# Kernel tuning notes

Hardware: AMD Instinct MI355X
Metric: run time of the kernel (lower is better)

Reference implementation:

```python
import jax, jax.numpy as jnp
import numpy as np

B, S, D, H, DQ, DM = 1, 2048, 1024, 16, 64, 4096
EPS = 1e-5
TEMPERATURE = 1.0


def layer_norm(x, gamma, beta):
    m = x.mean(-1, keepdims=True)
    v = jnp.mean((x - m) ** 2, axis=-1, keepdims=True)  # unbiased=False
    return gamma * (x - m) / jnp.sqrt(v + EPS) + beta


def setup_inputs() -> dict:
    key = jax.random.key(0)
    ks = jax.random.split(key, 12)
    w = lambda k, shape: jax.random.normal(k, shape, jnp.float32) * 0.02
    return {
        "E": jax.random.normal(ks[0], (B, S, D), jnp.float32),
        "mask": jnp.tril(jnp.ones((S, S), jnp.int32)),  # causal
        "W_Q": w(ks[1], (D, D)),
        "W_K": w(ks[2], (D, D)),
        "W_V": w(ks[3], (D, D)),
        "W_O": w(ks[4], (D, D)),
        "H_Q": w(ks[5], (H, DQ, D)),  # per-head Linear weights [out,in]
        "H_K": w(ks[6], (H, DQ, D)),
        "H_V": w(ks[7], (H, DQ, D)),
        "L1_w": w(ks[8], (DM, D)),
        "L1_b": jnp.zeros((DM,), jnp.float32),
        "L2_w": w(ks[9], (D, DM)),
        "L2_b": jnp.zeros((D,), jnp.float32),
        "gamma1": jnp.ones((D,), jnp.float32),
        "beta1": jnp.zeros((D,), jnp.float32),
        "gamma2": jnp.ones((D,), jnp.float32),
        "beta2": jnp.zeros((D,), jnp.float32),
    }


def reference(E, mask, W_Q, W_K, W_V, W_O, H_Q, H_K, H_V,
              L1_w, L1_b, L2_w, L2_b, gamma1, beta1, gamma2, beta2):
    # --- multi-head attention (dropout omitted: inference/eval) ---
    Q = E @ W_Q.T  # [B,S,D]
    K = E @ W_K.T
    V = E @ W_V.T
    # per-head projections (vectorized over the torch per-head Linear loop)
    q = jnp.einsum('bsd,hed->bhse', Q, H_Q)  # [B,H,S,DQ]
    k = jnp.einsum('bsd,hed->bhse', K, H_K)
    v = jnp.einsum('bsd,hed->bhse', V, H_V)
    scores = jnp.einsum('bhse,bhte->bhst', q, k) / jnp.sqrt(jnp.float32(DQ))
    scores = jnp.where(mask == 0, jnp.float32(-1e9), scores)
    weights = jax.nn.softmax(scores, axis=-1) / TEMPERATURE
    o = jnp.einsum('bhst,bhte->bhse', weights, v)        # [B,H,S,DQ]
    o = o.transpose(0, 2, 1, 3).reshape(E.shape[0], E.shape[1], D)  # concat heads
    att = o @ W_O.T
    # residual 1: E + Norm(sublayer(E))  (norm applied to sublayer output)
    x1 = E + layer_norm(att, gamma1, beta1)
    # --- MLP ---
    mlp = jax.nn.relu(x1 @ L1_w.T + L1_b) @ L2_w.T + L2_b
    return x1 + layer_norm(mlp, gamma2, beta2)
```

## Files before the change

### kernel.cpp

```cpp
#include <hip/hip_runtime.h>
#include <hip/hip_bf16.h>
#include <stdint.h>
#include <stddef.h>

typedef __attribute__((ext_vector_type(8))) short bf16x8;
typedef __attribute__((ext_vector_type(4))) short short4v;
typedef __attribute__((ext_vector_type(4))) float f32x4;

#define DEV static __device__ __forceinline__

DEV float bf2f(short s) {
  union { unsigned int u; float f; } c;
  c.u = ((unsigned int)(unsigned short)s) << 16;
  return c.f;
}
DEV short f2bf(float f) {
  union { float f; unsigned int u; } c; c.f = f;
  c.u += 0x7fffu + ((c.u >> 16) & 1);
  return (short)(c.u >> 16);
}
DEV unsigned int cvtpk_bf16(float lo, float hi) {
  unsigned int r;
  asm("v_cvt_pk_bf16_f32 %0, %1, %2" : "=v"(r) : "v"(lo), "v"(hi));
  return r;
}

struct CvtJob { const float* src; short* dst; int n4; };
struct CvtArgs { CvtJob j[8]; int n; };

__global__ __launch_bounds__(256) void cvt_kernel(CvtArgs a) {
  int tid = blockIdx.x * blockDim.x + threadIdx.x;
  int stride = gridDim.x * blockDim.x;
  for (int jj = 0; jj < a.n; ++jj) {
    const float4* s = (const float4*)a.j[jj].src;
    short4v* d = (short4v*)a.j[jj].dst;
    int n4 = a.j[jj].n4;
    for (int i = tid; i < n4; i += stride) {
      float4 v = s[i];
      short4v o = { f2bf(v.x), f2bf(v.y), f2bf(v.z), f2bf(v.w) };
      d[i] = o;
    }
  }
}

struct TcvtArgs { const float* src[3]; short* dst[3]; };

__global__ __launch_bounds__(256) void tcvt_kernel(TcvtArgs a) {
  __shared__ float tile[64][65];
  int z = blockIdx.z;
  const float* src = a.src[z];
  short* dst = a.dst[z];
  int bi = blockIdx.x * 64;
  int bj = blockIdx.y * 64;
  int t = threadIdx.x;
  int r0 = t >> 4;
  int c4 = (t & 15) * 4;
  #pragma unroll
  for (int rr = 0; rr < 4; ++rr) {
    int r = rr * 16 + r0;
    float4 v = *(const float4*)&src[(size_t)(bi + r) * 1024 + bj + c4];
    tile[r][c4] = v.x; tile[r][c4 + 1] = v.y; tile[r][c4 + 2] = v.z; tile[r][c4 + 3] = v.w;
  }
  __syncthreads();
  #pragma unroll
  for (int ww = 0; ww < 4; ++ww) {
    int orow = ww * 16 + r0;
    short4v o = { f2bf(tile[c4][orow]), f2bf(tile[c4 + 1][orow]),
                  f2bf(tile[c4 + 2][orow]), f2bf(tile[c4 + 3][orow]) };
    *(short4v*)&dst[(size_t)(bj + orow) * 1024 + bi + c4] = o;
  }
}

struct GemmArgs {
  const short* A[4];
  const short* B[4];
  void* C[4];
  const float* bias;
  int M, N, K, klen, kbase_step;
};

template<int EPI>
__global__ __launch_bounds__(256) void gemm_bt(GemmArgs g) {
  __shared__ alignas(16) short As[2][128 * 64];
  __shared__ alignas(16) short Bs[2][128 * 64];
  int z = blockIdx.z;
  const short* A = g.A[z];
  const short* B = g.B[z];
  int kb = z * g.kbase_step;

  int bx = blockIdx.x, by = blockIdx.y;
  int tid = threadIdx.x;
  int lane = tid & 63, wid = tid >> 6;
  int l15 = lane & 15, l4 = lane >> 4;
  int wr = (wid >> 1) * 64, wc = (wid & 1) * 64;
  int K = g.K, N = g.N;

  const short* Ab = A + (size_t)(by * 128) * K + kb;
  const short* Bb = B + (size_t)(bx * 128) * K + kb;

  int sR = lane >> 3;
  int sC = ((lane & 7) ^ sR) * 8;

  auto stage = [&](int buf, int k0) {
    const short* Abk = Ab + k0;
    const short* Bbk = Bb + k0;
    #pragma unroll
    for (int i = 0; i < 4; ++i) {
      int rbase = (wid * 4 + i) * 8;
      __builtin_amdgcn_global_load_lds(
          (const __attribute__((address_space(1))) void*)(Abk + (size_t)(rbase + sR) * K + sC),
          (__attribute__((address_space(3))) void*)&As[buf][rbase * 64], 16, 0, 0);
      __builtin_amdgcn_global_load_lds(
          (const __attribute__((address_space(1))) void*)(Bbk + (size_t)(rbase + sR) * K + sC),
          (__attribute__((address_space(3))) void*)&Bs[buf][rbase * 64], 16, 0, 0);
    }
  };

  f32x4 acc[4][4] = {};

  stage(0, 0);
  int cur = 0;

  for (int k0 = 0; k0 < g.klen; k0 += 64) {
    if (k0 + 64 < g.klen) {
      stage(cur ^ 1, k0 + 64);
      asm volatile("s_waitcnt vmcnt(8)" ::: "memory");
    } else {
      asm volatile("s_waitcnt vmcnt(0)" ::: "memory");
    }
    __builtin_amdgcn_s_barrier();

    bf16x8 af[2][4], bfr[2][4];
    int rj = l15 & 7;
    #pragma unroll
    for (int kk = 0; kk < 2; ++kk) {
      #pragma unroll
      for (int mi = 0; mi < 4; ++mi) {
        int r = wr + mi * 16 + l15;
        af[kk][mi] = *(const bf16x8*)&As[cur][r * 64 + (((kk << 2) | l4) ^ rj) * 8];
      }
      #pragma unroll
      for (int ni = 0; ni < 4; ++ni) {
        int r = wc + ni * 16 + l15;
        bfr[kk][ni] = *(const bf16x8*)&Bs[cur][r * 64 + (((kk << 2) | l4) ^ rj) * 8];
      }
    }
    #pragma unroll
    for (int kk = 0; kk < 2; ++kk)
      #pragma unroll
      for (int mi = 0; mi < 4; ++mi)
        #pragma unroll
        for (int ni = 0; ni < 4; ++ni)
          acc[mi][ni] = __builtin_amdgcn_mfma_f32_16x16x32_bf16(af[kk][mi], bfr[kk][ni], acc[mi][ni], 0, 0, 0);

    asm volatile("" ::: "memory");
    __builtin_amdgcn_s_barrier();
    cur ^= 1;
  }

  #pragma unroll
  for (int mi = 0; mi < 4; ++mi) {
    #pragma unroll
    for (int ni = 0; ni < 4; ++ni) {
      int col = bx * 128 + wc + ni * 16 + l15;
      float bv = 0.f;
      if (EPI == 1) bv = g.bias[col];
      bool ct = (EPI == 3) || (EPI == 4 && z == 2);
      if (ct) {
        int row0 = by * 128 + wr + mi * 16 + l4 * 4;
        short4v o4 = { f2bf(acc[mi][ni][0]), f2bf(acc[mi][ni][1]),
                       f2bf(acc[mi][ni][2]), f2bf(acc[mi][ni][3]) };
        *(short4v*)&((short*)g.C[z])[(size_t)col * g.M + row0] = o4;
      } else {
        #pragma unroll
        for (int j = 0; j < 4; ++j) {
          int row = by * 128 + wr + mi * 16 + l4 * 4 + j;
          float v = acc[mi][ni][j];
          if (EPI == 0 || EPI == 4) {
            ((short*)g.C[z])[(size_t)row * N + col] = f2bf(v);
          } else if (EPI == 1) {
            v = fmaxf(v + bv, 0.f);
            ((short*)g.C[z])[(size_t)row * N + col] = f2bf(v);
          } else {
            ((float*)g.C[z])[(size_t)row * N + col] = v;
          }
        }
      }
    }
  }
}

__global__ __launch_bounds__(256, 4) void flash_attn(
    const short* __restrict__ q, const short* __restrict__ k,
    const short* __restrict__ vt, short* __restrict__ o,
    float* __restrict__ Opart, float* __restrict__ Ml)
{
  const int HD = 1024, SS = 2048;
  int h = blockIdx.x;
  int cid = blockIdx.y;
  int qb = 0, cx = cid;
  while (cx >= (qb >> 3) + 1) { cx -= (qb >> 3) + 1; ++qb; }
  int nch = (qb >> 3) + 1;
  int tf = cx << 3;
  int tl = min(qb, tf + 7);
  int qbase = qb << 6;

  int tid = threadIdx.x;
  int wid = tid >> 6, lane = tid & 63;
  int l15 = lane & 15, l4 = lane >> 4;

  __shared__ alignas(16) short Ks[2][64 * 64];
  __shared__ alignas(16) short Vs[2][64 * 64];
  __shared__ alignas(16) char PsB[4][2048];

  bf16x8 qf[2];
  {
    int qr = qbase + wid * 16 + l15;
    const short* qp = q + (size_t)qr * HD + h * 64 + l4 * 8;
    bf16x8 r0 = *(const bf16x8*)qp;
    bf16x8 r1 = *(const bf16x8*)(qp + 32);
    const float SC = 0.1803368801f;
    #pragma unroll
    for (int j = 0; j < 8; ++j) {
      qf[0][j] = f2bf(bf2f(r0[j]) * SC);
      qf[1][j] = f2bf(bf2f(r1[j]) * SC);
    }
  }

  int sR = lane >> 3;
  int sC = (lane & 7) ^ sR;

  auto stage = [&](int buf, int t0) {
    const short* kbase = k + (size_t)t0 * HD + h * 64;
    const short* vbase = vt + (size_t)(h * 64) * SS + t0;
    #pragma unroll
    for (int i = 0; i < 2; ++i) {
      int rb = wid * 16 + i * 8;
      __builtin_amdgcn_global_load_lds(
          (const __attribute__((address_space(1))) void*)(kbase + (size_t)(rb + sR) * HD + sC * 8),
          (__attribute__((address_space(3))) void*)&Ks[buf][rb * 64], 16, 0, 0);
      __builtin_amdgcn_global_load_lds(
          (const __attribute__((address_space(1))) void*)(vbase + (size_t)(rb + sR) * SS + sC * 8),
          (__attribute__((address_space(3))) void*)&Vs[buf][rb * 64], 16, 0, 0);
    }
  };

  f32x4 oacc[4] = {};
  float mrun = -1e30f, lrun = 0.f;
  int q_g = qbase + wid * 16 + l15;
  int sbase = (lane & 48) + ((lane & 48) >> 2);

  char* Pw = &PsB[wid][l15 << 7];
  int swz = (l15 & 7) << 4;

  stage(0, tf << 6);
  int cur = 0;

  for (int tt = tf; tt <= tl; ++tt) {
    if (tt < tl) {
      stage(cur ^ 1, (tt + 1) << 6);
      asm volatile("s_waitcnt vmcnt(4)" ::: "memory");
    } else {
      asm volatile("s_waitcnt vmcnt(0)" ::: "memory");
    }
    __builtin_amdgcn_s_barrier();

    const short* KsB = &Ks[cur][0];
    const short* VsB = &Vs[cur][0];
    int t0 = tt << 6;

    f32x4 sc[4] = {};
    __builtin_amdgcn_s_setprio(1);
    #pragma unroll
    for (int ks = 0; ks < 2; ++ks)
      #pragma unroll
      for (int ns = 0; ns < 4; ++ns) {
        int r = ns * 16 + l15;
        bf16x8 kf = *(const bf16x8*)&KsB[r * 64 + (((ks << 2) | l4) ^ (r & 7)) * 8];
        sc[ns] = __builtin_amdgcn_mfma_f32_16x16x32_bf16(kf, qf[ks], sc[ns], 0, 0, 0);
      }
    __builtin_amdgcn_s_setprio(0);

    if (tt == qb) {
      #pragma unroll
      for (int ns = 0; ns < 4; ++ns)
        #pragma unroll
        for (int j = 0; j < 4; ++j) {
          int t_g = t0 + ns * 16 + l4 * 4 + j;
          if (t_g > q_g) sc[ns][j] = -1e30f;
        }
    }

    float mloc = sc[0][0];
    #pragma unroll
    for (int ns = 0; ns < 4; ++ns)
      #pragma unroll
      for (int j = 0; j < 4; ++j) mloc = fmaxf(mloc, sc[ns][j]);
    mloc = fmaxf(mloc, __shfl_xor(mloc, 16, 64));
    mloc = fmaxf(mloc, __shfl_xor(mloc, 32, 64));

    if (!__all(mloc - mrun <= 8.0f)) {
      float mnew = fmaxf(mrun, mloc);
      float sco = exp2f(mrun - mnew);
      float scR[4];
      #pragma unroll
      for (int j = 0; j < 4; ++j) scR[j] = __shfl(sco, sbase + j, 64);
      #pragma unroll
      for (int es = 0; es < 4; ++es)
        #pragma unroll
        for (int j = 0; j < 4; ++j) oacc[es][j] *= scR[j];
      lrun *= sco;
      mrun = mnew;
    }

    float psum = 0.f;
    float p[4][4];
    #pragma unroll
    for (int ns = 0; ns < 4; ++ns)
      #pragma unroll
      for (int j = 0; j < 4; ++j) {
        p[ns][j] = exp2f(sc[ns][j] - mrun);
        psum += p[ns][j];
      }
    psum += __shfl_xor(psum, 16, 64);
    psum += __shfl_xor(psum, 32, 64);
    lrun += psum;

    #pragma unroll
    for (int ns = 0; ns < 4; ++ns) {
      uint2 pv = { cvtpk_bf16(p[ns][0], p[ns][1]), cvtpk_bf16(p[ns][2], p[ns][3]) };
      *(uint2*)&Pw[((ns << 5) | (l4 << 3)) ^ swz] = pv;
    }

    __builtin_amdgcn_s_setprio(1);
    #pragma unroll
    for (int ks = 0; ks < 2; ++ks) {
      bf16x8 pf = *(const bf16x8*)&Pw[((ks << 6) | (l4 << 4)) ^ swz];
      #pragma unroll
      for (int es = 0; es < 4; ++es) {
        int r = es * 16 + l15;
        bf16x8 vf = *(const bf16x8*)&VsB[r * 64 + (((ks << 2) | l4) ^ (r & 7)) * 8];
        oacc[es] = __builtin_amdgcn_mfma_f32_16x16x32_bf16(pf, vf, oacc[es], 0, 0, 0);
      }
    }
    __builtin_amdgcn_s_setprio(0);

    asm volatile("" ::: "memory");
    __builtin_amdgcn_s_barrier();
    cur ^= 1;
  }

  if (nch == 1) {
    float linv = 1.f / lrun;
    float invR[4];
    #pragma unroll
    for (int j = 0; j < 4; ++j) invR[j] = __shfl(linv, sbase + j, 64);
    #pragma unroll
    for (int es = 0; es < 4; ++es)
      #pragma unroll
      for (int j = 0; j < 4; ++j) {
        int row = qbase + wid * 16 + l4 * 4 + j;
        o[(size_t)row * HD + h * 64 + es * 16 + l15] = f2bf(oacc[es][j] * invR[j]);
      }
  } else {
    size_t slot = (size_t)h * 80 + cid;
    float* op = Opart + slot * 4096;
    #pragma unroll
    for (int es = 0; es < 4; ++es)
      #pragma unroll
      for (int j = 0; j < 4; ++j) {
        int row = wid * 16 + l4 * 4 + j;
        op[row * 64 + es * 16 + l15] = oacc[es][j];
      }
    if (l4 == 0) {
      Ml[slot * 128 + wid * 16 + l15] = mrun;
      Ml[slot * 128 + 64 + wid * 16 + l15] = lrun;
    }
  }
}

__global__ __launch_bounds__(256) void attn_combine(
    const float* __restrict__ Opart, const float* __restrict__ Ml,
    short* __restrict__ o)
{
  const int HD = 1024;
  int h = blockIdx.x;
  int qb = 8 + blockIdx.y;
  int nch = (qb >> 3) + 1;
  int cb = 0;
  for (int qq = 0; qq < qb; ++qq) cb += (qq >> 3) + 1;
  int tid = threadIdx.x;
  int r = tid >> 2;
  int cq = (tid & 3) << 4;
  size_t slot0 = (size_t)h * 80 + cb;

  float mk[4], lk[4];
  float M = -1e30f;
  #pragma unroll
  for (int kk = 0; kk < 4; ++kk) {
    bool en = kk < nch;
    mk[kk] = en ? Ml[(slot0 + kk) * 128 + r] : -1e30f;
    lk[kk] = en ? Ml[(slot0 + kk) * 128 + 64 + r] : 0.f;
    M = fmaxf(M, mk[kk]);
  }
  float L = 0.f, w[4];
  #pragma unroll
  for (int kk = 0; kk < 4; ++kk) { w[kk] = exp2f(mk[kk] - M); L += w[kk] * lk[kk]; }

  float acc[16] = {};
  #pragma unroll
  for (int kk = 0; kk < 4; ++kk) {
    if (kk < nch) {
      const float* op = Opart + (slot0 + kk) * 4096 + r * 64 + cq;
      float wk = w[kk];
      #pragma unroll
      for (int c4 = 0; c4 < 4; ++c4) {
        float4 v = *(const float4*)&op[c4 * 4];
        acc[c4 * 4 + 0] += wk * v.x;
        acc[c4 * 4 + 1] += wk * v.y;
        acc[c4 * 4 + 2] += wk * v.z;
        acc[c4 * 4 + 3] += wk * v.w;
      }
    }
  }
  float inv = 1.f / L;
  int orow = (qb << 6) + r;
  short* dst = o + (size_t)orow * HD + h * 64 + cq;
  #pragma unroll
  for (int c4 = 0; c4 < 4; ++c4) {
    short4v ov = { f2bf(acc[c4 * 4 + 0] * inv), f2bf(acc[c4 * 4 + 1] * inv),
                   f2bf(acc[c4 * 4 + 2] * inv), f2bf(acc[c4 * 4 + 3] * inv) };
    *(short4v*)&dst[c4 * 4] = ov;
  }
}

__global__ __launch_bounds__(256) void ln_res1(
    const float* __restrict__ P0, const float* __restrict__ P1,
    const float* __restrict__ P2, const float* __restrict__ P3,
    const float* __restrict__ E,
    const float* __restrict__ gamma, const float* __restrict__ beta,
    float* __restrict__ x1f, short* __restrict__ x1b)
{
  int row = blockIdx.x, tid = threadIdx.x;
  int lane = tid & 63, wid = tid >> 6;
  size_t idx = (size_t)row * 1024 + tid * 4;
  float4 p0 = *(const float4*)&P0[idx];
  float4 p1 = *(const float4*)&P1[idx];
  float4 p2 = *(const float4*)&P2[idx];
  float4 p3 = *(const float4*)&P3[idx];
  float a[4] = { p0.x + p1.x + p2.x + p3.x, p0.y + p1.y + p2.y + p3.y,
                 p0.z + p1.z + p2.z + p3.z, p0.w + p1.w + p2.w + p3.w };
  float s = a[0] + a[1] + a[2] + a[3];
  float q = a[0]*a[0] + a[1]*a[1] + a[2]*a[2] + a[3]*a[3];
  #pragma unroll
  for (int off = 1; off < 64; off <<= 1) { s += __shfl_xor(s, off, 64); q += __shfl_xor(q, off, 64); }
  __shared__ float red[8];
  if (lane == 0) { red[wid] = s; red[4 + wid] = q; }
  __syncthreads();
  s = red[0] + red[1] + red[2] + red[3];
  q = red[4] + red[5] + red[6] + red[7];
  float mean = s * (1.f / 1024.f);
  float var = q * (1.f / 1024.f) - mean * mean;
  float rstd = rsqrtf(var + 1e-5f);
  float4 ev = *(const float4*)&E[idx];
  float4 gv = *(const float4*)&gamma[tid * 4];
  float4 bv = *(const float4*)&beta[tid * 4];
  float o0 = ev.x + gv.x * (a[0] - mean) * rstd + bv.x;
  float o1 = ev.y + gv.y * (a[1] - mean) * rstd + bv.y;
  float o2 = ev.z + gv.z * (a[2] - mean) * rstd + bv.z;
  float o3 = ev.w + gv.w * (a[3] - mean) * rstd + bv.w;
  float4 xo = { o0, o1, o2, o3 };
  *(float4*)&x1f[idx] = xo;
  short4v xb = { f2bf(o0), f2bf(o1), f2bf(o2), f2bf(o3) };
  *(short4v*)&x1b[idx] = xb;
}

__global__ __launch_bounds__(256) void ln_res2(
    const float* __restrict__ M0, const float* __restrict__ M1,
    const float* __restrict__ M2, const float* __restrict__ M3,
    const float* __restrict__ bias, const float* __restrict__ x1f,
    const float* __restrict__ gamma, const float* __restrict__ beta,
    float* __restrict__ out)
{
  int row = blockIdx.x, tid = threadIdx.x;
  int lane = tid & 63, wid = tid >> 6;
  size_t idx = (size_t)row * 1024 + tid * 4;
  float4 m0 = *(const float4*)&M0[idx];
  float4 m1 = *(const float4*)&M1[idx];
  float4 m2 = *(const float4*)&M2[idx];
  float4 m3 = *(const float4*)&M3[idx];
  float4 bb = *(const float4*)&bias[tid * 4];
  float a[4] = { m0.x + m1.x + m2.x + m3.x + bb.x,
                 m0.y + m1.y + m2.y + m3.y + bb.y,
                 m0.z + m1.z + m2.z + m3.z + bb.z,
                 m0.w + m1.w + m2.w + m3.w + bb.w };
  float s = a[0] + a[1] + a[2] + a[3];
  float q = a[0]*a[0] + a[1]*a[1] + a[2]*a[2] + a[3]*a[3];
  #pragma unroll
  for (int off = 1; off < 64; off <<= 1) { s += __shfl_xor(s, off, 64); q += __shfl_xor(q, off, 64); }
  __shared__ float red[8];
  if (lane == 0) { red[wid] = s; red[4 + wid] = q; }
  __syncthreads();
  s = red[0] + red[1] + red[2] + red[3];
  q = red[4] + red[5] + red[6] + red[7];
  float mean = s * (1.f / 1024.f);
  float var = q * (1.f / 1024.f) - mean * mean;
  float rstd = rsqrtf(var + 1e-5f);
  float4 xv = *(const float4*)&x1f[idx];
  float4 gv = *(const float4*)&gamma[tid * 4];
  float4 bv = *(const float4*)&beta[tid * 4];
  float4 ov = { xv.x + gv.x * (a[0] - mean) * rstd + bv.x,
                xv.y + gv.y * (a[1] - mean) * rstd + bv.y,
                xv.z + gv.z * (a[2] - mean) * rstd + bv.z,
                xv.w + gv.w * (a[3] - mean) * rstd + bv.w };
  *(float4*)&out[idx] = ov;
}

extern "C" void kernel_launch(void* const* d_in, const int* in_sizes, int n_in,
                              void* d_out, int out_size, void* d_ws, size_t ws_size,
                              hipStream_t stream)
{
  (void)in_sizes; (void)n_in; (void)out_size;
  const int S = 2048, D = 1024, DM = 4096, H = 16;
  const size_t MB = 1u << 20;
  const float* E   = (const float*)d_in[0];
  const float* W_Q = (const float*)d_in[2];
  const float* W_K = (const float*)d_in[3];
  const float* W_V = (const float*)d_in[4];
  const float* W_O = (const float*)d_in[5];
  const float* H_Q = (const float*)d_in[6];
  const float* H_K = (const float*)d_in[7];
  const float* H_V = (const float*)d_in[8];
  const float* L1w = (const float*)d_in[9];
  const float* L1b = (const float*)d_in[10];
  const float* L2w = (const float*)d_in[11];
  const float* L2b = (const float*)d_in[12];
  const float* g1  = (const float*)d_in[13];
  const float* b1  = (const float*)d_in[14];
  const float* g2  = (const float*)d_in[15];
  const float* b2  = (const float*)d_in[16];

  char* base = (char*)d_ws;
  if (ws_size < 90 * MB) return;

  short* Ebf  = (short*)(base + 0 * MB);
  short* TWq  = (short*)(base + 4 * MB);
  short* TWk  = (short*)(base + 6 * MB);
  short* TWv  = (short*)(base + 8 * MB);
  short* Wob  = (short*)(base + 10 * MB);
  short* Hqb  = (short*)(base + 12 * MB);
  short* Hkb  = (short*)(base + 14 * MB);
  short* Hvb  = (short*)(base + 16 * MB);
  short* L1wb = (short*)(base + 18 * MB);
  short* L2wb = (short*)(base + 26 * MB);
  short* Cq   = (short*)(base + 34 * MB);
  short* Ck   = (short*)(base + 36 * MB);
  short* Cv   = (short*)(base + 38 * MB);
  short* qh   = (short*)(base + 46 * MB);
  short* kh   = (short*)(base + 50 * MB);
  short* vtb  = (short*)(base + 54 * MB);
  short* obuf = (short*)(base + 58 * MB);
  short* x1b  = (short*)(base + 62 * MB);
  float* x1f  = (float*)(base + 66 * MB);
  short* hbuf = (short*)(base + 74 * MB);
  float* WOP0 = (float*)(base + 74 * MB);
  float* WOP1 = (float*)(base + 82 * MB);
  float* WOP2 = (float*)(base + 34 * MB);
  float* WOP3 = (float*)(base + 42 * MB);
  float* MP0  = (float*)(base + 34 * MB);
  float* MP1  = (float*)(base + 42 * MB);
  float* MP2  = (float*)(base + 50 * MB);
  float* MP3  = (float*)(base + 58 * MB);
  float* Opart = (float*)(base + 66 * MB);
  float* Ml    = (float*)(base + 86 * MB);

  CvtArgs ca;
  ca.j[0] = { E,   Ebf,  S * D / 4 };
  ca.j[1] = { W_O, Wob,  D * D / 4 };
  ca.j[2] = { H_Q, Hqb,  D * D / 4 };
  ca.j[3] = { H_K, Hkb,  D * D / 4 };
  ca.j[4] = { H_V, Hvb,  D * D / 4 };
  ca.j[5] = { L1w, L1wb, DM * D / 4 };
  ca.j[6] = { L2w, L2wb, DM * D / 4 };
  ca.n = 7;
  cvt_kernel<<<2048, 256, 0, stream>>>(ca);

  TcvtArgs ta;
  ta.src[0] = W_Q; ta.src[1] = W_K; ta.src[2] = W_V;
  ta.dst[0] = TWq; ta.dst[1] = TWk; ta.dst[2] = TWv;
  tcvt_kernel<<<dim3(16, 16, 3), 256, 0, stream>>>(ta);

  GemmArgs ga;

  ga = {};
  ga.A[0] = Hqb; ga.A[1] = Hkb; ga.A[2] = Hvb;
  ga.B[0] = TWq; ga.B[1] = TWk; ga.B[2] = TWv;
  ga.C[0] = Cq;  ga.C[1] = Ck;  ga.C[2] = Cv;
  ga.M = D; ga.N = D; ga.K = D; ga.klen = D; ga.kbase_step = 0;
  gemm_bt<0><<<dim3(D / 128, D / 128, 3), 256, 0, stream>>>(ga);

  ga = {};
  ga.A[0] = Ebf; ga.A[1] = Ebf; ga.A[2] = Ebf;
  ga.B[0] = Cq;  ga.B[1] = Ck;  ga.B[2] = Cv;
  ga.C[0] = qh;  ga.C[1] = kh;  ga.C[2] = vtb;
  ga.M = S; ga.N = D; ga.K = D; ga.klen = D; ga.kbase_step = 0;
  gemm_bt<4><<<dim3(D / 128, S / 128, 3), 256, 0, stream>>>(ga);

  flash_attn<<<dim3(H, 80), 256, 0, stream>>>(qh, kh, vtb, obuf, Opart, Ml);
  attn_combine<<<dim3(H, 24), 256, 0, stream>>>(Opart, Ml, obuf);

  ga = {};
  ga.A[0] = obuf; ga.A[1] = obuf; ga.A[2] = obuf; ga.A[3] = obuf;
  ga.B[0] = Wob;  ga.B[1] = Wob;  ga.B[2] = Wob;  ga.B[3] = Wob;
  ga.C[0] = WOP0; ga.C[1] = WOP1; ga.C[2] = WOP2; ga.C[3] = WOP3;
  ga.M = S; ga.N = D; ga.K = D; ga.klen = D / 4; ga.kbase_step = D / 4;
  gemm_bt<2><<<dim3(D / 128, S / 128, 4), 256, 0, stream>>>(ga);

  ln_res1<<<S, 256, 0, stream>>>(WOP0, WOP1, WOP2, WOP3, E, g1, b1, x1f, x1b);

  ga = {};
  ga.A[0] = x1b; ga.B[0] = L1wb; ga.C[0] = hbuf;
  ga.bias = L1b;
  ga.M = S; ga.N = DM; ga.K = D; ga.klen = D; ga.kbase_step = 0;
  gemm_bt<1><<<dim3(DM / 128, S / 128, 1), 256, 0, stream>>>(ga);

  ga = {};
  ga.A[0] = hbuf; ga.A[1] = hbuf; ga.A[2] = hbuf; ga.A[3] = hbuf;
  ga.B[0] = L2wb; ga.B[1] = L2wb; ga.B[2] = L2wb; ga.B[3] = L2wb;
  ga.C[0] = MP0;  ga.C[1] = MP1;  ga.C[2] = MP2;  ga.C[3] = MP3;
  ga.M = S; ga.N = D; ga.K = DM; ga.klen = DM / 4; ga.kbase_step = DM / 4;
  gemm_bt<2><<<dim3(D / 128, S / 128, 4), 256, 0, stream>>>(ga);

  ln_res2<<<S, 256, 0, stream>>>(MP0, MP1, MP2, MP3, L2b, x1f, g2, b2, (float*)d_out);
}
```

Before: 176.6 us.

## Store split-K and attention partials in bf16 and merge prep kernels

```diff
diff --git a/kernel.cpp b/kernel.cpp
--- a/kernel.cpp
+++ b/kernel.cpp
@@ -26,48 +26,52 @@
 }
 
 struct CvtJob { const float* src; short* dst; int n4; };
-struct CvtArgs { CvtJob j[8]; int n; };
-
-__global__ __launch_bounds__(256) void cvt_kernel(CvtArgs a) {
-  int tid = blockIdx.x * blockDim.x + threadIdx.x;
-  int stride = gridDim.x * blockDim.x;
-  for (int jj = 0; jj < a.n; ++jj) {
-    const float4* s = (const float4*)a.j[jj].src;
-    short4v* d = (short4v*)a.j[jj].dst;
-    int n4 = a.j[jj].n4;
-    for (int i = tid; i < n4; i += stride) {
-      float4 v = s[i];
-      short4v o = { f2bf(v.x), f2bf(v.y), f2bf(v.z), f2bf(v.w) };
-      d[i] = o;
-    }
-  }
-}
-
-struct TcvtArgs { const float* src[3]; short* dst[3]; };
-
-__global__ __launch_bounds__(256) void tcvt_kernel(TcvtArgs a) {
+struct PrepArgs {
+  CvtJob j[8]; int n;
+  const float* tsrc[3]; short* tdst[3];
+};
+
+__global__ __launch_bounds__(256) void prep_kernel(PrepArgs a) {
   __shared__ float tile[64][65];
-  int z = blockIdx.z;
-  const float* src = a.src[z];
-  short* dst = a.dst[z];
-  int bi = blockIdx.x * 64;
-  int bj = blockIdx.y * 64;
-  int t = threadIdx.x;
-  int r0 = t >> 4;
-  int c4 = (t & 15) * 4;
-  #pragma unroll
-  for (int rr = 0; rr < 4; ++rr) {
-    int r = rr * 16 + r0;
-    float4 v = *(const float4*)&src[(size_t)(bi + r) * 1024 + bj + c4];
-    tile[r][c4] = v.x; tile[r][c4 + 1] = v.y; tile[r][c4 + 2] = v.z; tile[r][c4 + 3] = v.w;
-  }
-  __syncthreads();
-  #pragma unroll
-  for (int ww = 0; ww < 4; ++ww) {
-    int orow = ww * 16 + r0;
-    short4v o = { f2bf(tile[c4][orow]), f2bf(tile[c4 + 1][orow]),
-                  f2bf(tile[c4 + 2][orow]), f2bf(tile[c4 + 3][orow]) };
-    *(short4v*)&dst[(size_t)(bj + orow) * 1024 + bi + c4] = o;
+  int bx = blockIdx.x;
+  if (bx < 2048) {
+    int tid = bx * 256 + threadIdx.x;
+    int stride = 2048 * 256;
+    for (int jj = 0; jj < a.n; ++jj) {
+      const float4* s = (const float4*)a.j[jj].src;
+      short4v* d = (short4v*)a.j[jj].dst;
+      int n4 = a.j[jj].n4;
+      for (int i = tid; i < n4; i += stride) {
+        float4 v = s[i];
+        short4v o = { f2bf(v.x), f2bf(v.y), f2bf(v.z), f2bf(v.w) };
+        d[i] = o;
+      }
+    }
+  } else {
+    int id = bx - 2048;
+    int z = id >> 8;
+    int rem = id & 255;
+    const float* src = a.tsrc[z];
+    short* dst = a.tdst[z];
+    int bi = (rem >> 4) * 64;
+    int bj = (rem & 15) * 64;
+    int t = threadIdx.x;
+    int r0 = t >> 4;
+    int c4 = (t & 15) * 4;
+    #pragma unroll
+    for (int rr = 0; rr < 4; ++rr) {
+      int r = rr * 16 + r0;
+      float4 v = *(const float4*)&src[(size_t)(bi + r) * 1024 + bj + c4];
+      tile[r][c4] = v.x; tile[r][c4 + 1] = v.y; tile[r][c4 + 2] = v.z; tile[r][c4 + 3] = v.w;
+    }
+    __syncthreads();
+    #pragma unroll
+    for (int ww = 0; ww < 4; ++ww) {
+      int orow = ww * 16 + r0;
+      short4v o = { f2bf(tile[c4][orow]), f2bf(tile[c4 + 1][orow]),
+                    f2bf(tile[c4 + 2][orow]), f2bf(tile[c4 + 3][orow]) };
+      *(short4v*)&dst[(size_t)(bj + orow) * 1024 + bi + c4] = o;
+    }
   }
 }
 
@@ -182,7 +186,7 @@
             v = fmaxf(v + bv, 0.f);
             ((short*)g.C[z])[(size_t)row * N + col] = f2bf(v);
           } else {
-            ((float*)g.C[z])[(size_t)row * N + col] = v;
+            ((short*)g.C[z])[(size_t)row * N + col] = f2bf(v);
           }
         }
       }
@@ -193,7 +197,7 @@
 __global__ __launch_bounds__(256, 4) void flash_attn(
     const short* __restrict__ q, const short* __restrict__ k,
     const short* __restrict__ vt, short* __restrict__ o,
-    float* __restrict__ Opart, float* __restrict__ Ml)
+    short* __restrict__ Opart, float* __restrict__ Ml)
 {
   const int HD = 1024, SS = 2048;
   int h = blockIdx.x;
@@ -364,13 +368,13 @@
       }
   } else {
     size_t slot = (size_t)h * 80 + cid;
-    float* op = Opart + slot * 4096;
+    short* op = Opart + slot * 4096;
     #pragma unroll
     for (int es = 0; es < 4; ++es)
       #pragma unroll
       for (int j = 0; j < 4; ++j) {
         int row = wid * 16 + l4 * 4 + j;
-        op[row * 64 + es * 16 + l15] = oacc[es][j];
+        op[row * 64 + es * 16 + l15] = f2bf(oacc[es][j]);
       }
     if (l4 == 0) {
       Ml[slot * 128 + wid * 16 + l15] = mrun;
@@ -380,7 +384,7 @@
 }
 
 __global__ __launch_bounds__(256) void attn_combine(
-    const float* __restrict__ Opart, const float* __restrict__ Ml,
+    const short* __restrict__ Opart, const float* __restrict__ Ml,
     short* __restrict__ o)
 {
   const int HD = 1024;
@@ -411,15 +415,15 @@
   #pragma unroll
   for (int kk = 0; kk < 4; ++kk) {
     if (kk < nch) {
-      const float* op = Opart + (slot0 + kk) * 4096 + r * 64 + cq;
+      const short* op = Opart + (slot0 + kk) * 4096 + r * 64 + cq;
       float wk = w[kk];
       #pragma unroll
       for (int c4 = 0; c4 < 4; ++c4) {
-        float4 v = *(const float4*)&op[c4 * 4];
-        acc[c4 * 4 + 0] += wk * v.x;
-        acc[c4 * 4 + 1] += wk * v.y;
-        acc[c4 * 4 + 2] += wk * v.z;
-        acc[c4 * 4 + 3] += wk * v.w;
+        short4v v = *(const short4v*)&op[c4 * 4];
+        acc[c4 * 4 + 0] += wk * bf2f(v[0]);
+        acc[c4 * 4 + 1] += wk * bf2f(v[1]);
+        acc[c4 * 4 + 2] += wk * bf2f(v[2]);
+        acc[c4 * 4 + 3] += wk * bf2f(v[3]);
       }
     }
   }
@@ -435,8 +439,8 @@
 }
 
 __global__ __launch_bounds__(256) void ln_res1(
-    const float* __restrict__ P0, const float* __restrict__ P1,
-    const float* __restrict__ P2, const float* __restrict__ P3,
+    const short* __restrict__ P0, const short* __restrict__ P1,
+    const short* __restrict__ P2, const short* __restrict__ P3,
     const float* __restrict__ E,
     const float* __restrict__ gamma, const float* __restrict__ beta,
     float* __restrict__ x1f, short* __restrict__ x1b)
@@ -444,12 +448,14 @@
   int row = blockIdx.x, tid = threadIdx.x;
   int lane = tid & 63, wid = tid >> 6;
   size_t idx = (size_t)row * 1024 + tid * 4;
-  float4 p0 = *(const float4*)&P0[idx];
-  float4 p1 = *(const float4*)&P1[idx];
-  float4 p2 = *(const float4*)&P2[idx];
-  float4 p3 = *(const float4*)&P3[idx];
-  float a[4] = { p0.x + p1.x + p2.x + p3.x, p0.y + p1.y + p2.y + p3.y,
-                 p0.z + p1.z + p2.z + p3.z, p0.w + p1.w + p2.w + p3.w };
+  short4v p0 = *(const short4v*)&P0[idx];
+  short4v p1 = *(const short4v*)&P1[idx];
+  short4v p2 = *(const short4v*)&P2[idx];
+  short4v p3 = *(const short4v*)&P3[idx];
+  float a[4];
+  #pragma unroll
+  for (int j = 0; j < 4; ++j)
+    a[j] = bf2f(p0[j]) + bf2f(p1[j]) + bf2f(p2[j]) + bf2f(p3[j]);
   float s = a[0] + a[1] + a[2] + a[3];
   float q = a[0]*a[0] + a[1]*a[1] + a[2]*a[2] + a[3]*a[3];
   #pragma unroll
@@ -476,8 +482,8 @@
 }
 
 __global__ __launch_bounds__(256) void ln_res2(
-    const float* __restrict__ M0, const float* __restrict__ M1,
-    const float* __restrict__ M2, const float* __restrict__ M3,
+    const short* __restrict__ M0, const short* __restrict__ M1,
+    const short* __restrict__ M2, const short* __restrict__ M3,
     const float* __restrict__ bias, const float* __restrict__ x1f,
     const float* __restrict__ gamma, const float* __restrict__ beta,
     float* __restrict__ out)
@@ -485,15 +491,16 @@
   int row = blockIdx.x, tid = threadIdx.x;
   int lane = tid & 63, wid = tid >> 6;
   size_t idx = (size_t)row * 1024 + tid * 4;
-  float4 m0 = *(const float4*)&M0[idx];
-  float4 m1 = *(const float4*)&M1[idx];
-  float4 m2 = *(const float4*)&M2[idx];
-  float4 m3 = *(const float4*)&M3[idx];
+  short4v m0 = *(const short4v*)&M0[idx];
+  short4v m1 = *(const short4v*)&M1[idx];
+  short4v m2 = *(const short4v*)&M2[idx];
+  short4v m3 = *(const short4v*)&M3[idx];
   float4 bb = *(const float4*)&bias[tid * 4];
-  float a[4] = { m0.x + m1.x + m2.x + m3.x + bb.x,
-                 m0.y + m1.y + m2.y + m3.y + bb.y,
-                 m0.z + m1.z + m2.z + m3.z + bb.z,
-                 m0.w + m1.w + m2.w + m3.w + bb.w };
+  float a[4];
+  a[0] = bf2f(m0[0]) + bf2f(m1[0]) + bf2f(m2[0]) + bf2f(m3[0]) + bb.x;
+  a[1] = bf2f(m0[1]) + bf2f(m1[1]) + bf2f(m2[1]) + bf2f(m3[1]) + bb.y;
+  a[2] = bf2f(m0[2]) + bf2f(m1[2]) + bf2f(m2[2]) + bf2f(m3[2]) + bb.z;
+  a[3] = bf2f(m0[3]) + bf2f(m1[3]) + bf2f(m2[3]) + bf2f(m3[3]) + bb.w;
   float s = a[0] + a[1] + a[2] + a[3];
   float q = a[0]*a[0] + a[1]*a[1] + a[2]*a[2] + a[3]*a[3];
   #pragma unroll
@@ -563,32 +570,29 @@
   short* x1b  = (short*)(base + 62 * MB);
   float* x1f  = (float*)(base + 66 * MB);
   short* hbuf = (short*)(base + 74 * MB);
-  float* WOP0 = (float*)(base + 74 * MB);
-  float* WOP1 = (float*)(base + 82 * MB);
-  float* WOP2 = (float*)(base + 34 * MB);
-  float* WOP3 = (float*)(base + 42 * MB);
-  float* MP0  = (float*)(base + 34 * MB);
-  float* MP1  = (float*)(base + 42 * MB);
-  float* MP2  = (float*)(base + 50 * MB);
-  float* MP3  = (float*)(base + 58 * MB);
-  float* Opart = (float*)(base + 66 * MB);
+  short* WOP0 = (short*)(base + 74 * MB);
+  short* WOP1 = (short*)(base + 82 * MB);
+  short* WOP2 = (short*)(base + 34 * MB);
+  short* WOP3 = (short*)(base + 42 * MB);
+  short* MP0  = (short*)(base + 34 * MB);
+  short* MP1  = (short*)(base + 42 * MB);
+  short* MP2  = (short*)(base + 50 * MB);
+  short* MP3  = (short*)(base + 58 * MB);
+  short* Opart = (short*)(base + 66 * MB);
   float* Ml    = (float*)(base + 86 * MB);
 
-  CvtArgs ca;
-  ca.j[0] = { E,   Ebf,  S * D / 4 };
-  ca.j[1] = { W_O, Wob,  D * D / 4 };
-  ca.j[2] = { H_Q, Hqb,  D * D / 4 };
-  ca.j[3] = { H_K, Hkb,  D * D / 4 };
-  ca.j[4] = { H_V, Hvb,  D * D / 4 };
-  ca.j[5] = { L1w, L1wb, DM * D / 4 };
-  ca.j[6] = { L2w, L2wb, DM * D / 4 };
-  ca.n = 7;
-  cvt_kernel<<<2048, 256, 0, stream>>>(ca);
-
-  TcvtArgs ta;
-  ta.src[0] = W_Q; ta.src[1] = W_K; ta.src[2] = W_V;
-  ta.dst[0] = TWq; ta.dst[1] = TWk; ta.dst[2] = TWv;
-  tcvt_kernel<<<dim3(16, 16, 3), 256, 0, stream>>>(ta);
+  PrepArgs pa;
+  pa.j[0] = { E,   Ebf,  S * D / 4 };
+  pa.j[1] = { W_O, Wob,  D * D / 4 };
+  pa.j[2] = { H_Q, Hqb,  D * D / 4 };
+  pa.j[3] = { H_K, Hkb,  D * D / 4 };
+  pa.j[4] = { H_V, Hvb,  D * D / 4 };
+  pa.j[5] = { L1w, L1wb, DM * D / 4 };
+  pa.j[6] = { L2w, L2wb, DM * D / 4 };
+  pa.n = 7;
+  pa.tsrc[0] = W_Q; pa.tsrc[1] = W_K; pa.tsrc[2] = W_V;
+  pa.tdst[0] = TWq; pa.tdst[1] = TWk; pa.tdst[2] = TWv;
+  prep_kernel<<<2048 + 768, 256, 0, stream>>>(pa);
 
   GemmArgs ga;
 
```

Result: faster. 168.9 us (-4.4%).
